# Kernel optimization log

Measured on AMD Instinct MI355X. Metric: run time of the kernel, lower is better.

Reference implementation:

```python
import jax, jax.numpy as jnp
import numpy as np
import math

V, D, L, M, S, B = 32000, 1024, 4, 4096, 2048, 4


def sinusoidal_positional_encoding(max_seq_len, embedding_dim):
    position = jnp.arange(max_seq_len, dtype=jnp.float32)[:, None]
    div_term = jnp.exp(jnp.arange(0, embedding_dim, 2, dtype=jnp.float32)
                       * (-math.log(10000.0) / embedding_dim))
    pe = jnp.zeros((max_seq_len, embedding_dim), jnp.float32)
    pe = pe.at[:, 0::2].set(jnp.sin(position * div_term))
    pe = pe.at[:, 1::2].set(jnp.cos(position * div_term))
    return pe


def setup_inputs() -> dict:
    key = jax.random.key(0)
    ks = jax.random.split(key, 12)
    s = 0.02
    return {
        "x": jax.random.randint(ks[0], (B, S), 0, V, dtype=jnp.int64),
        "emb": jax.random.normal(ks[1], (V, D), jnp.float32) * s,
        "pos_enc": sinusoidal_positional_encoding(S, D),
        "wq": jax.random.normal(ks[2], (D, D), jnp.float32) * s,
        "bq": jnp.zeros((D,), jnp.float32),
        "wk": jax.random.normal(ks[3], (D, D), jnp.float32) * s,
        "bk": jnp.zeros((D,), jnp.float32),
        "wv": jax.random.normal(ks[4], (D, D), jnp.float32) * s,
        "bv": jnp.zeros((D,), jnp.float32),
        "w1s": jax.random.normal(ks[5], (L, D, M), jnp.float32) * s,
        "b1s": jnp.zeros((L, M), jnp.float32),
        "w2s": jax.random.normal(ks[6], (L, M, D), jnp.float32) * s,
        "b2s": jnp.zeros((L, D), jnp.float32),
    }


def reference(x, emb, pos_enc, wq, bq, wk, bk, wv, bv, w1s, b1s, w2s, b2s):
    seq = x.shape[1]
    h = emb[x] + pos_enc[:seq]                      # [B,S,D]
    q = h @ wq + bq
    k = h @ wk + bk
    v = h @ wv + bv
    scores = jnp.einsum('bqd,bkd->bqk', q, k) / jnp.sqrt(jnp.float32(k.shape[-1]))
    # Faithful to source: triu(diagonal=0) KEPT -> attends to self and future.
    mask = jnp.triu(jnp.ones((seq, seq), bool), k=0)
    scores = jnp.where(mask, scores, -jnp.inf)
    attn = jax.nn.softmax(scores, axis=-1)
    h = jax.nn.relu(jnp.einsum('bqk,bkd->bqd', attn, v))
    for i in range(w1s.shape[0]):
        h = jax.nn.relu(h @ w1s[i] + b1s[i])
        h = jax.nn.relu(h @ w2s[i] + b2s[i])
    return h
```

## Files before the change

kernel.cpp:

```cpp
#include <hip/hip_runtime.h>

#define D_DIM 1024
#define S_DIM 2048
#define B_DIM 4
#define M_DIM 4096
#define NTOK  8192

typedef unsigned short u16;
typedef __attribute__((ext_vector_type(8))) short short8;
typedef __attribute__((ext_vector_type(4))) float fx4;

static __device__ __forceinline__ float b2f(u16 u) {
  union { unsigned int i; float f; } v; v.i = ((unsigned int)u) << 16; return v.f;
}
static __device__ __forceinline__ u16 f2b(float f) {
  union { float f; unsigned int i; } v; v.f = f;
  unsigned int r = v.i + 0x7fffu + ((v.i >> 16) & 1u);
  return (u16)(r >> 16);
}
static __device__ __forceinline__ void async16(u16* lds, const u16* g) {
  __builtin_amdgcn_global_load_lds(
      (__attribute__((address_space(1))) void*)(u16*)g,
      (__attribute__((address_space(3))) void*)lds, 16, 0, 0);
}

__global__ void canary_kernel(float* __restrict__ out) {
  const long i = ((long)blockIdx.x * 256 + threadIdx.x) * 4;
  float4 v = {1.0f, 1.0f, 1.0f, 1.0f};
  *(float4*)(out + i) = v;
}

__global__ void Transformer_33792802685820_kernel(
    const int* __restrict__ x, const float* __restrict__ emb,
    const float* __restrict__ pe, u16* __restrict__ h) {
  const int t = blockIdx.x;
  const int s = t & (S_DIM - 1);
  const int row = x[t];
  const int d = threadIdx.x * 4;
  float4 e = *(const float4*)(emb + (long)row * D_DIM + d);
  float4 p = *(const float4*)(pe + (long)s * D_DIM + d);
  ushort4 o;
  o.x = f2b(e.x + p.x);
  o.y = f2b(e.y + p.y);
  o.z = f2b(e.z + p.z);
  o.w = f2b(e.w + p.w);
  *(ushort4*)(h + (long)t * D_DIM + d) = o;
}

__global__ void transpose_f_kernel(
    const float* __restrict__ in, u16* __restrict__ out, int R, int C) {
  __shared__ float tile[32][33];
  const int c0 = blockIdx.x * 32, r0 = blockIdx.y * 32;
  const int tx = threadIdx.x, ty = threadIdx.y;
  for (int i = ty; i < 32; i += 8)
    tile[i][tx] = in[(long)(r0 + i) * C + (c0 + tx)];
  __syncthreads();
  for (int i = ty; i < 32; i += 8)
    out[(long)(c0 + i) * R + (r0 + tx)] = f2b(tile[tx][i]);
}

__global__ void transpose_b_kernel(
    const u16* __restrict__ in, u16* __restrict__ out, int R, int C) {
  __shared__ u16 tile[32][33];
  const long zoff = (long)blockIdx.z * R * C;
  const int c0 = blockIdx.x * 32, r0 = blockIdx.y * 32;
  const int tx = threadIdx.x, ty = threadIdx.y;
  for (int i = ty; i < 32; i += 8)
    tile[i][tx] = in[zoff + (long)(r0 + i) * C + (c0 + tx)];
  __syncthreads();
  for (int i = ty; i < 32; i += 8)
    out[zoff + (long)(c0 + i) * R + (r0 + tx)] = tile[tx][i];
}

template<bool RELU, bool BIAS, bool OUTF32>
__global__ void gemm_bt(
    const u16* __restrict__ A, const u16* __restrict__ Bt,
    const float* __restrict__ bias, u16* __restrict__ C, float* __restrict__ Cf,
    int M, int N, int K, float scale, long sA, long sB, long sC) {
  __shared__ u16 As[128 * 32];
  __shared__ u16 Bs[128 * 32];
  const int tid  = threadIdx.x;
  const int wave = tid >> 6;
  const int lane = tid & 63;
  const int quad = lane >> 4;
  const int l16  = lane & 15;
  const int wm = (wave & 1) << 6;
  const int wn = (wave >> 1) << 6;
  A  += (long)blockIdx.z * sA;
  Bt += (long)blockIdx.z * sB;
  const int m0 = blockIdx.y << 7;
  const int n0 = blockIdx.x << 7;

  const int row_a = tid >> 2;
  const int c4    = (tid & 3) << 3;
  const u16* gA = A  + (long)(m0 + row_a) * K + c4;
  const u16* gB = Bt + (long)(n0 + row_a) * K + c4;
  u16* lA = &As[tid * 8];
  u16* lB = &Bs[tid * 8];

  fx4 acc[4][4] = {};

  for (int k0 = 0; k0 < K; k0 += 32) {
    async16(lA,            gA + k0);
    async16(lA + 64 * 32,  gA + (long)64 * K + k0);
    async16(lB,            gB + k0);
    async16(lB + 64 * 32,  gB + (long)64 * K + k0);
    __syncthreads();
    short8 af[4], bfv[4];
    #pragma unroll
    for (int i = 0; i < 4; ++i) {
      af[i]  = *(const short8*)&As[(wm + i * 16 + l16) * 32 + quad * 8];
      bfv[i] = *(const short8*)&Bs[(wn + i * 16 + l16) * 32 + quad * 8];
    }
    __syncthreads();
    #pragma unroll
    for (int mi = 0; mi < 4; ++mi)
      #pragma unroll
      for (int ni = 0; ni < 4; ++ni)
        acc[mi][ni] = __builtin_amdgcn_mfma_f32_16x16x32_bf16(
            af[mi], bfv[ni], acc[mi][ni], 0, 0, 0);
  }

  float bv[4];
  #pragma unroll
  for (int ni = 0; ni < 4; ++ni)
    bv[ni] = BIAS ? bias[n0 + wn + ni * 16 + l16] : 0.0f;

  #pragma unroll
  for (int mi = 0; mi < 4; ++mi) {
    #pragma unroll
    for (int r = 0; r < 4; ++r) {
      const long row = m0 + wm + mi * 16 + quad * 4 + r;
      const long base = row * N + n0 + wn + l16;
      #pragma unroll
      for (int ni = 0; ni < 4; ++ni) {
        float v = acc[mi][ni][r] * scale + bv[ni];
        if (RELU) { if (v < 0.0f) v = 0.0f; }
        if (OUTF32) Cf[(long)blockIdx.z * sC + base + ni * 16] = v;
        else        C [(long)blockIdx.z * sC + base + ni * 16] = f2b(v);
      }
    }
  }
}

__global__ void softmax_kernel(u16* __restrict__ P) {
  const int q = blockIdx.x;
  u16* p = P + ((long)blockIdx.y * S_DIM + q) * S_DIM;
  const int tid = threadIdx.x;
  const int wave = tid >> 6, lane = tid & 63;
  __shared__ float red[4];
  float vals[8];
  float mx = -3.0e38f;
  for (int it = 0; it < 8; ++it) {
    int k = tid + it * 256;
    float v = (k >= q) ? b2f(p[k]) : -3.0e38f;
    vals[it] = v;
    mx = fmaxf(mx, v);
  }
  for (int off = 32; off > 0; off >>= 1)
    mx = fmaxf(mx, __shfl_down(mx, off, 64));
  if (lane == 0) red[wave] = mx;
  __syncthreads();
  mx = fmaxf(fmaxf(red[0], red[1]), fmaxf(red[2], red[3]));
  __syncthreads();
  float sum = 0.0f;
  for (int it = 0; it < 8; ++it) {
    int k = tid + it * 256;
    float e = (k >= q) ? __expf(vals[it] - mx) : 0.0f;
    vals[it] = e;
    sum += e;
  }
  for (int off = 32; off > 0; off >>= 1)
    sum += __shfl_down(sum, off, 64);
  if (lane == 0) red[wave] = sum;
  __syncthreads();
  sum = red[0] + red[1] + red[2] + red[3];
  const float inv = 1.0f / sum;
  for (int it = 0; it < 8; ++it) {
    int k = tid + it * 256;
    p[k] = f2b(vals[it] * inv);
  }
}

extern "C" void kernel_launch(void* const* d_in, const int* in_sizes, int n_in,
                              void* d_out, int out_size, void* d_ws, size_t ws_size,
                              hipStream_t stream) {
  (void)in_sizes; (void)n_in; (void)out_size; (void)ws_size;
  const int*   x   = (const int*)d_in[0];
  const float* emb = (const float*)d_in[1];
  const float* pe  = (const float*)d_in[2];
  const float* wq  = (const float*)d_in[3];
  const float* bq  = (const float*)d_in[4];
  const float* wk  = (const float*)d_in[5];
  const float* bk  = (const float*)d_in[6];
  const float* wv  = (const float*)d_in[7];
  const float* bv  = (const float*)d_in[8];
  const float* w1s = (const float*)d_in[9];
  const float* b1s = (const float*)d_in[10];
  const float* w2s = (const float*)d_in[11];
  const float* b2s = (const float*)d_in[12];
  float* out = (float*)d_out;

  u16* ws  = (u16*)d_ws;
  u16* h   = ws;
  u16* q   = h  + (long)NTOK * D_DIM;
  u16* kx  = q  + (long)NTOK * D_DIM;
  u16* v   = kx + (long)NTOK * D_DIM;
  u16* P   = v  + (long)NTOK * D_DIM;
  u16* wqT = P  + (long)B_DIM * S_DIM * S_DIM;
  u16* wkT = wqT + (long)D_DIM * D_DIM;
  u16* wvT = wkT + (long)D_DIM * D_DIM;
  u16* w1T = wvT + (long)D_DIM * D_DIM;
  u16* w2T = w1T + (long)D_DIM * M_DIM;
  u16* vT  = q;
  u16* mb  = kx;

  const dim3 blk256(256);
  const dim3 blkT(32, 8);

  canary_kernel<<<dim3(NTOK), blk256, 0, stream>>>(out);

  transpose_f_kernel<<<dim3(32, 32), blkT, 0, stream>>>(wq, wqT, 1024, 1024);
  transpose_f_kernel<<<dim3(32, 32), blkT, 0, stream>>>(wk, wkT, 1024, 1024);
  transpose_f_kernel<<<dim3(32, 32), blkT, 0, stream>>>(wv, wvT, 1024, 1024);

  Transformer_33792802685820_kernel<<<dim3(NTOK), blk256, 0, stream>>>(x, emb, pe, h);

  gemm_bt<false, true, false><<<dim3(8, 64, 1), blk256, 0, stream>>>(h, wqT, bq, q,  nullptr, NTOK, D_DIM, D_DIM, 1.0f, 0, 0, 0);
  gemm_bt<false, true, false><<<dim3(8, 64, 1), blk256, 0, stream>>>(h, wkT, bk, kx, nullptr, NTOK, D_DIM, D_DIM, 1.0f, 0, 0, 0);
  gemm_bt<false, true, false><<<dim3(8, 64, 1), blk256, 0, stream>>>(h, wvT, bv, v,  nullptr, NTOK, D_DIM, D_DIM, 1.0f, 0, 0, 0);

  gemm_bt<false, false, false><<<dim3(16, 16, 4), blk256, 0, stream>>>(q, kx, nullptr, P, nullptr,
      S_DIM, S_DIM, D_DIM, 0.03125f, (long)S_DIM * D_DIM, (long)S_DIM * D_DIM, (long)S_DIM * S_DIM);

  softmax_kernel<<<dim3(S_DIM, B_DIM), blk256, 0, stream>>>(P);

  transpose_b_kernel<<<dim3(32, 64, 4), blkT, 0, stream>>>(v, vT, 2048, 1024);
  gemm_bt<true, false, false><<<dim3(8, 16, 4), blk256, 0, stream>>>(P, vT, nullptr, h, nullptr,
      S_DIM, D_DIM, S_DIM, 1.0f, (long)S_DIM * S_DIM, (long)D_DIM * S_DIM, (long)S_DIM * D_DIM);

  for (int i = 0; i < 4; ++i) {
    transpose_f_kernel<<<dim3(128, 32), blkT, 0, stream>>>(w1s + (long)i * D_DIM * M_DIM, w1T, 1024, 4096);
    transpose_f_kernel<<<dim3(32, 128), blkT, 0, stream>>>(w2s + (long)i * D_DIM * M_DIM, w2T, 4096, 1024);
    gemm_bt<true, true, false><<<dim3(32, 64, 1), blk256, 0, stream>>>(
        h, w1T, b1s + i * M_DIM, mb, nullptr, NTOK, M_DIM, D_DIM, 1.0f, 0, 0, 0);
    if (i == 3)
      gemm_bt<true, true, true><<<dim3(8, 64, 1), blk256, 0, stream>>>(
          mb, w2T, b2s + i * D_DIM, nullptr, out, NTOK, D_DIM, M_DIM, 1.0f, 0, 0, 0);
    else
      gemm_bt<true, true, false><<<dim3(8, 64, 1), blk256, 0, stream>>>(
          mb, w2T, b2s + i * D_DIM, h, nullptr, NTOK, D_DIM, M_DIM, 1.0f, 0, 0, 0);
  }
}
```

Baseline: 1.234 ms.

## Add 256x256-tile 512-thread GEMM with ping-pong scheduling for projection and MLP

Adds a new GEMM kernel that computes 256x256 output tiles with 8 waves. It double-buffers LDS through async global-to-LDS loads, uses an XOR-swizzled layout, and interleaves barrier-separated MFMA clusters at raised priority with the next tile's loads. A workgroup remap groups tiles into chunks of eight for cache locality. All QKV, score and MLP GEMMs switch to it to raise arithmetic intensity and overlap memory with compute. The cost is more LDS and registers per block, fewer blocks for the smaller GEMMs, and many barriers.

```diff
diff --git a/kernel.cpp b/kernel.cpp
--- a/kernel.cpp
+++ b/kernel.cpp
@@ -23,6 +23,9 @@
       (__attribute__((address_space(1))) void*)(u16*)g,
       (__attribute__((address_space(3))) void*)lds, 16, 0, 0);
 }
+
+#define FENCE asm volatile("" ::: "memory")
+#define BARR  do { FENCE; __builtin_amdgcn_s_barrier(); FENCE; } while (0)
 
 __global__ void canary_kernel(float* __restrict__ out) {
   const long i = ((long)blockIdx.x * 256 + threadIdx.x) * 4;
@@ -143,6 +146,137 @@
   }
 }
 
+template<bool RELU, bool BIAS, bool OUTF32>
+__global__ __launch_bounds__(512, 2) void gemm256(
+    const u16* __restrict__ A, const u16* __restrict__ Bt,
+    const float* __restrict__ bias, u16* __restrict__ C, float* __restrict__ Cf,
+    int M, int N, int K, float scale, long sA_, long sB_, long sC_) {
+  __shared__ u16 sA[2][256 * 64];
+  __shared__ u16 sB[2][256 * 64];
+  const int tid  = threadIdx.x;
+  const int lane = tid & 63;
+  const int wave = tid >> 6;
+  const int quad = lane >> 4;
+  const int l16  = lane & 15;
+  const int swz  = l16 & 7;
+  const int wm   = wave >> 2;
+  const int wn   = wave & 3;
+
+  const int gx  = gridDim.x;
+  const int nwg = gx * gridDim.y;
+  const int id0 = blockIdx.y * gx + blockIdx.x;
+  const int cpx = nwg >> 3;
+  const int sid = (id0 & 7) * cpx + (id0 >> 3);
+  const int n0  = (sid % gx) << 8;
+  const int m0  = (sid / gx) << 8;
+
+  A  += (long)blockIdx.z * sA_;
+  Bt += (long)blockIdx.z * sB_;
+
+  const int srow = tid >> 3;
+  const int cl   = (tid & 7) ^ (srow & 7);
+  const u16* gA = A  + (long)(m0 + srow) * K + cl * 8;
+  const u16* gB = Bt + (long)(n0 + srow) * K + cl * 8;
+  const int ldst = tid * 8;
+
+  fx4 acc[8][4] = {};
+  short8 ar[4], br[4];
+
+  const int NT = K >> 6;
+
+#define STAGE_A(b, t, half) do { \
+    const long ko_ = (long)(t) * 64; \
+    async16(&sA[b][(half) * 8192 + ldst],        gA + (long)((half) * 128     ) * K + ko_); \
+    async16(&sA[b][(half) * 8192 + 4096 + ldst], gA + (long)((half) * 128 + 64) * K + ko_); \
+  } while (0)
+#define STAGE_B(b, t, half) do { \
+    const long ko_ = (long)(t) * 64; \
+    async16(&sB[b][(half) * 8192 + ldst],        gB + (long)((half) * 128     ) * K + ko_); \
+    async16(&sB[b][(half) * 8192 + 4096 + ldst], gB + (long)((half) * 128 + 64) * K + ko_); \
+  } while (0)
+#define RD_A(b, mh, ks) do { \
+    _Pragma("unroll") for (int i_ = 0; i_ < 4; ++i_) { \
+      const int row_ = wm * 128 + ((mh) * 4 + i_) * 16 + l16; \
+      ar[i_] = *(const short8*)&sA[b][row_ * 64 + ((((ks) << 2) | quad) ^ swz) * 8]; \
+    } } while (0)
+#define RD_B(b, ks) do { \
+    _Pragma("unroll") for (int n_ = 0; n_ < 4; ++n_) { \
+      const int row_ = wn * 64 + n_ * 16 + l16; \
+      br[n_] = *(const short8*)&sB[b][row_ * 64 + ((((ks) << 2) | quad) ^ swz) * 8]; \
+    } } while (0)
+#define MM(mh) do { \
+    _Pragma("unroll") for (int i_ = 0; i_ < 4; ++i_) \
+      _Pragma("unroll") for (int n_ = 0; n_ < 4; ++n_) \
+        acc[(mh) * 4 + i_][n_] = __builtin_amdgcn_mfma_f32_16x16x32_bf16( \
+            ar[i_], br[n_], acc[(mh) * 4 + i_][n_], 0, 0, 0); \
+  } while (0)
+#define MFMA_CLUSTER(mh) do { \
+    __builtin_amdgcn_sched_barrier(0); \
+    __builtin_amdgcn_s_setprio(1); \
+    MM(mh); \
+    __builtin_amdgcn_s_setprio(0); \
+    __builtin_amdgcn_sched_barrier(0); \
+  } while (0)
+
+  STAGE_B(0, 0, 0); STAGE_B(0, 0, 1);
+  STAGE_A(0, 0, 0); STAGE_A(0, 0, 1);
+  STAGE_B(1, 1, 0);
+  asm volatile("s_waitcnt vmcnt(2)" ::: "memory");
+  BARR;
+
+  for (int t = 0; t < NT; ++t) {
+    const int b = t & 1, b1 = b ^ 1;
+    RD_A(b, 0, 0); RD_B(b, 0);
+    if (t + 1 < NT) STAGE_B(b1, t + 1, 1);
+    BARR;
+    MFMA_CLUSTER(0);
+    BARR;
+    RD_A(b, 1, 0);
+    if (t + 1 < NT) STAGE_A(b1, t + 1, 0);
+    BARR;
+    MFMA_CLUSTER(1);
+    BARR;
+    RD_A(b, 0, 1); RD_B(b, 1);
+    if (t + 1 < NT) STAGE_A(b1, t + 1, 1);
+    BARR;
+    MFMA_CLUSTER(0);
+    BARR;
+    RD_A(b, 1, 1);
+    if (t + 2 < NT) STAGE_B(b, t + 2, 0);
+    BARR;
+    MFMA_CLUSTER(1);
+    asm volatile("s_waitcnt vmcnt(2)" ::: "memory");
+    BARR;
+  }
+
+  float bv[4];
+  #pragma unroll
+  for (int n = 0; n < 4; ++n)
+    bv[n] = BIAS ? bias[n0 + wn * 64 + n * 16 + l16] : 0.0f;
+
+  #pragma unroll
+  for (int f = 0; f < 8; ++f) {
+    #pragma unroll
+    for (int r = 0; r < 4; ++r) {
+      const long row  = m0 + wm * 128 + f * 16 + quad * 4 + r;
+      const long base = (long)blockIdx.z * sC_ + row * N + n0 + wn * 64 + l16;
+      #pragma unroll
+      for (int n = 0; n < 4; ++n) {
+        float v = acc[f][n][r] * scale + bv[n];
+        if (RELU) { if (v < 0.0f) v = 0.0f; }
+        if (OUTF32) Cf[base + n * 16] = v;
+        else        C [base + n * 16] = f2b(v);
+      }
+    }
+  }
+#undef STAGE_A
+#undef STAGE_B
+#undef RD_A
+#undef RD_B
+#undef MM
+#undef MFMA_CLUSTER
+}
+
 __global__ void softmax_kernel(u16* __restrict__ P) {
   const int q = blockIdx.x;
   u16* p = P + ((long)blockIdx.y * S_DIM + q) * S_DIM;
@@ -216,6 +350,7 @@
   u16* mb  = kx;
 
   const dim3 blk256(256);
+  const dim3 blk512(512);
   const dim3 blkT(32, 8);
 
   canary_kernel<<<dim3(NTOK), blk256, 0, stream>>>(out);
@@ -226,11 +361,11 @@
 
   Transformer_33792802685820_kernel<<<dim3(NTOK), blk256, 0, stream>>>(x, emb, pe, h);
 
-  gemm_bt<false, true, false><<<dim3(8, 64, 1), blk256, 0, stream>>>(h, wqT, bq, q,  nullptr, NTOK, D_DIM, D_DIM, 1.0f, 0, 0, 0);
-  gemm_bt<false, true, false><<<dim3(8, 64, 1), blk256, 0, stream>>>(h, wkT, bk, kx, nullptr, NTOK, D_DIM, D_DIM, 1.0f, 0, 0, 0);
-  gemm_bt<false, true, false><<<dim3(8, 64, 1), blk256, 0, stream>>>(h, wvT, bv, v,  nullptr, NTOK, D_DIM, D_DIM, 1.0f, 0, 0, 0);
-
-  gemm_bt<false, false, false><<<dim3(16, 16, 4), blk256, 0, stream>>>(q, kx, nullptr, P, nullptr,
+  gemm256<false, true, false><<<dim3(4, 32, 1), blk512, 0, stream>>>(h, wqT, bq, q,  nullptr, NTOK, D_DIM, D_DIM, 1.0f, 0, 0, 0);
+  gemm256<false, true, false><<<dim3(4, 32, 1), blk512, 0, stream>>>(h, wkT, bk, kx, nullptr, NTOK, D_DIM, D_DIM, 1.0f, 0, 0, 0);
+  gemm256<false, true, false><<<dim3(4, 32, 1), blk512, 0, stream>>>(h, wvT, bv, v,  nullptr, NTOK, D_DIM, D_DIM, 1.0f, 0, 0, 0);
+
+  gemm256<false, false, false><<<dim3(8, 8, 4), blk512, 0, stream>>>(q, kx, nullptr, P, nullptr,
       S_DIM, S_DIM, D_DIM, 0.03125f, (long)S_DIM * D_DIM, (long)S_DIM * D_DIM, (long)S_DIM * S_DIM);
 
   softmax_kernel<<<dim3(S_DIM, B_DIM), blk256, 0, stream>>>(P);
@@ -242,13 +377,13 @@
   for (int i = 0; i < 4; ++i) {
     transpose_f_kernel<<<dim3(128, 32), blkT, 0, stream>>>(w1s + (long)i * D_DIM * M_DIM, w1T, 1024, 4096);
     transpose_f_kernel<<<dim3(32, 128), blkT, 0, stream>>>(w2s + (long)i * D_DIM * M_DIM, w2T, 4096, 1024);
-    gemm_bt<true, true, false><<<dim3(32, 64, 1), blk256, 0, stream>>>(
+    gemm256<true, true, false><<<dim3(16, 32, 1), blk512, 0, stream>>>(
         h, w1T, b1s + i * M_DIM, mb, nullptr, NTOK, M_DIM, D_DIM, 1.0f, 0, 0, 0);
     if (i == 3)
-      gemm_bt<true, true, true><<<dim3(8, 64, 1), blk256, 0, stream>>>(
+      gemm256<true, true, true><<<dim3(4, 32, 1), blk512, 0, stream>>>(
           mb, w2T, b2s + i * D_DIM, nullptr, out, NTOK, D_DIM, M_DIM, 1.0f, 0, 0, 0);
     else
-      gemm_bt<true, true, false><<<dim3(8, 64, 1), blk256, 0, stream>>>(
+      gemm256<true, true, false><<<dim3(4, 32, 1), blk512, 0, stream>>>(
           mb, w2T, b2s + i * D_DIM, h, nullptr, NTOK, D_DIM, M_DIM, 1.0f, 0, 0, 0);
   }
 }
```

Result: no change. 1.255 ms (+1.7%).

## Add 256x256-tile 8-wave pipelined GEMM for QK^T and FFN up-projection

Applied to the files above, without the earlier changes.

Introduces a new bf16 MFMA GEMM kernel with 256x256 output tiles, 512 threads, double-buffered LDS filled by async global-to-LDS loads, an interleaved stage/compute schedule with barriers and wave priority boosts, and an XCD-aware block remap. It replaces the 128-tile kernel for the QK^T score GEMM and the FFN first GEMM. The aim is more data reuse per block and load latency hidden behind MFMA work. The cost is fewer blocks, which can leave compute units underfilled on the smaller grids, plus heavy LDS and register use.

```diff
diff --git a/kernel.cpp b/kernel.cpp
--- a/kernel.cpp
+++ b/kernel.cpp
@@ -143,6 +143,141 @@
   }
 }
 
+template<bool RELU, bool BIAS, bool OUTF32>
+__global__ __launch_bounds__(512) void gemm256(
+    const u16* __restrict__ A, const u16* __restrict__ Bt,
+    const float* __restrict__ bias, u16* __restrict__ C, float* __restrict__ Cf,
+    int M, int N, int K, float scale, long sA_, long sB_, long sC_) {
+  __shared__ u16 sA[2][16384];
+  __shared__ u16 sB[2][16384];
+  const int tid  = threadIdx.x;
+  const int lane = tid & 63;
+  const int wave = tid >> 6;
+  const int quad = lane >> 4;
+  const int l16  = lane & 15;
+  const int wm   = wave >> 2;
+  const int wn   = wave & 3;
+
+  const int gx  = gridDim.x;
+  const int nwg = gx * gridDim.y;
+  const int id0 = blockIdx.y * gx + blockIdx.x;
+  const int cpx = nwg >> 3;
+  const int sid = (id0 & 7) * cpx + (id0 >> 3);
+  const int n0  = (sid % gx) << 8;
+  const int m0  = (sid / gx) << 8;
+
+  A  += (long)blockIdx.z * sA_;
+  Bt += (long)blockIdx.z * sB_;
+
+  const int lr   = tid >> 2;
+  const int pc   = tid & 3;
+  const int lc   = pc ^ (lr & 3);
+  const int arow = (lr & 63) + ((lr >> 6) << 7);
+  const u16* gA0 = A  + (long)(m0 + arow) * K + lc * 8;
+  const u16* gB0 = Bt + (long)(n0 + lr)   * K + lc * 8;
+  const int ldst = tid << 3;
+
+  const int rdo = (quad ^ (l16 & 3)) << 3;
+  const int raA = wm * 64 + l16;
+  const int raB = wn * 64 + l16;
+
+  fx4 acc[8][4] = {};
+  short8 ar[4], br[4];
+
+  const int NT = K >> 6;
+
+#define STG_A(b, t, mh, ks) \
+  async16(&sA[b][((((ks) << 1) | (mh)) << 12) + ldst], \
+          gA0 + (long)(mh) * 64 * K + (long)(t) * 64 + (ks) * 32)
+#define STG_B1(b, t, ks) \
+  async16(&sB[b][((ks) << 13) + ldst], gB0 + (long)(t) * 64 + (ks) * 32)
+#define STG_B2(b, t, ks) \
+  async16(&sB[b][((ks) << 13) + 4096 + ldst], \
+          gB0 + (long)128 * K + (long)(t) * 64 + (ks) * 32)
+#define RD_A(b, mh, ks) do { \
+    _Pragma("unroll") for (int i_ = 0; i_ < 4; ++i_) \
+      ar[i_] = *(const short8*)&sA[b][((((ks) << 1) | (mh)) << 12) + (raA + i_ * 16) * 32 + rdo]; \
+  } while (0)
+#define RD_B(b, ks) do { \
+    _Pragma("unroll") for (int n_ = 0; n_ < 4; ++n_) \
+      br[n_] = *(const short8*)&sB[b][((ks) << 13) + (raB + n_ * 16) * 32 + rdo]; \
+  } while (0)
+#define PRIO_MM(mh) do { \
+    __builtin_amdgcn_s_setprio(1); \
+    _Pragma("unroll") for (int i_ = 0; i_ < 4; ++i_) \
+      _Pragma("unroll") for (int n_ = 0; n_ < 4; ++n_) \
+        acc[(mh) * 4 + i_][n_] = __builtin_amdgcn_mfma_f32_16x16x32_bf16( \
+            ar[i_], br[n_], acc[(mh) * 4 + i_][n_], 0, 0, 0); \
+    __builtin_amdgcn_s_setprio(0); \
+  } while (0)
+#define SBAR  __builtin_amdgcn_s_barrier()
+#define SCHED __builtin_amdgcn_sched_barrier(0)
+
+  STG_A(0, 0, 0, 0); STG_B1(0, 0, 0); STG_B2(0, 0, 0); STG_A(0, 0, 1, 0);
+  STG_A(0, 0, 0, 1); STG_B1(0, 0, 1); STG_B2(0, 0, 1); STG_A(0, 0, 1, 1);
+  STG_A(1, 1, 0, 0); STG_B1(1, 1, 0); STG_B2(1, 1, 0); STG_A(1, 1, 1, 0);
+  STG_A(1, 1, 0, 1); STG_B1(1, 1, 1);
+  asm volatile("s_waitcnt vmcnt(6)");
+  SCHED;
+  SBAR;
+
+  for (int t = 0; t < NT; ++t) {
+    const int b = t & 1, b1 = b ^ 1;
+    RD_A(b, 0, 0); RD_B(b, 0);
+    if (t + 1 < NT) { STG_B2(b1, t + 1, 1); STG_A(b1, t + 1, 1, 1); }
+    SBAR;
+    PRIO_MM(0);
+    SBAR; SCHED;
+    RD_A(b, 1, 0);
+    if (t + 2 < NT) { STG_A(b, t + 2, 0, 0); STG_B1(b, t + 2, 0); }
+    SBAR;
+    PRIO_MM(1);
+    SBAR; SCHED;
+    RD_A(b, 0, 1); RD_B(b, 1);
+    if (t + 2 < NT) { STG_B2(b, t + 2, 0); STG_A(b, t + 2, 1, 0); }
+    SBAR;
+    PRIO_MM(0);
+    SBAR; SCHED;
+    RD_A(b, 1, 1);
+    if (t + 2 < NT) { STG_A(b, t + 2, 0, 1); STG_B1(b, t + 2, 1); }
+    SBAR;
+    PRIO_MM(1);
+    if (t + 2 < NT) asm volatile("s_waitcnt vmcnt(6)");
+    else            asm volatile("s_waitcnt vmcnt(0)");
+    SCHED;
+    SBAR; SCHED;
+  }
+
+  float bv[4];
+  #pragma unroll
+  for (int n = 0; n < 4; ++n)
+    bv[n] = BIAS ? bias[n0 + wn * 64 + n * 16 + l16] : 0.0f;
+
+  #pragma unroll
+  for (int f = 0; f < 8; ++f) {
+    #pragma unroll
+    for (int r = 0; r < 4; ++r) {
+      const long row  = m0 + wm * 128 + f * 16 + quad * 4 + r;
+      const long base = (long)blockIdx.z * sC_ + row * N + n0 + wn * 64 + l16;
+      #pragma unroll
+      for (int n = 0; n < 4; ++n) {
+        float v = acc[f][n][r] * scale + bv[n];
+        if (RELU) { if (v < 0.0f) v = 0.0f; }
+        if (OUTF32) Cf[base + n * 16] = v;
+        else        C [base + n * 16] = f2b(v);
+      }
+    }
+  }
+#undef STG_A
+#undef STG_B1
+#undef STG_B2
+#undef RD_A
+#undef RD_B
+#undef PRIO_MM
+#undef SBAR
+#undef SCHED
+}
+
 __global__ void softmax_kernel(u16* __restrict__ P) {
   const int q = blockIdx.x;
   u16* p = P + ((long)blockIdx.y * S_DIM + q) * S_DIM;
@@ -216,6 +351,7 @@
   u16* mb  = kx;
 
   const dim3 blk256(256);
+  const dim3 blk512(512);
   const dim3 blkT(32, 8);
 
   canary_kernel<<<dim3(NTOK), blk256, 0, stream>>>(out);
@@ -230,7 +366,7 @@
   gemm_bt<false, true, false><<<dim3(8, 64, 1), blk256, 0, stream>>>(h, wkT, bk, kx, nullptr, NTOK, D_DIM, D_DIM, 1.0f, 0, 0, 0);
   gemm_bt<false, true, false><<<dim3(8, 64, 1), blk256, 0, stream>>>(h, wvT, bv, v,  nullptr, NTOK, D_DIM, D_DIM, 1.0f, 0, 0, 0);
 
-  gemm_bt<false, false, false><<<dim3(16, 16, 4), blk256, 0, stream>>>(q, kx, nullptr, P, nullptr,
+  gemm256<false, false, false><<<dim3(8, 8, 4), blk512, 0, stream>>>(q, kx, nullptr, P, nullptr,
       S_DIM, S_DIM, D_DIM, 0.03125f, (long)S_DIM * D_DIM, (long)S_DIM * D_DIM, (long)S_DIM * S_DIM);
 
   softmax_kernel<<<dim3(S_DIM, B_DIM), blk256, 0, stream>>>(P);
@@ -242,7 +378,7 @@
   for (int i = 0; i < 4; ++i) {
     transpose_f_kernel<<<dim3(128, 32), blkT, 0, stream>>>(w1s + (long)i * D_DIM * M_DIM, w1T, 1024, 4096);
     transpose_f_kernel<<<dim3(32, 128), blkT, 0, stream>>>(w2s + (long)i * D_DIM * M_DIM, w2T, 4096, 1024);
-    gemm_bt<true, true, false><<<dim3(32, 64, 1), blk256, 0, stream>>>(
+    gemm256<true, true, false><<<dim3(16, 32, 1), blk512, 0, stream>>>(
         h, w1T, b1s + i * M_DIM, mb, nullptr, NTOK, M_DIM, D_DIM, 1.0f, 0, 0, 0);
     if (i == 3)
       gemm_bt<true, true, true><<<dim3(8, 64, 1), blk256, 0, stream>>>(
```

New measurement: 1.240 ms. No clear change (+0.4%).

## Replace GEMM with 256-row double-buffered swizzled LDS kernel using 512 threads

Applied to the files above, without the earlier changes.

Replaces the 128x128, BK=32, single-buffered GEMM with a 256xBN (BN 128/256), BK=64 tile kernel run by 512 threads. It double-buffers LDS with async global-to-LDS loads, uses an XOR swizzle on LDS columns to avoid bank conflicts, raises wave priority around the MFMA bursts, and remaps block IDs so neighbouring tiles are grouped (intended for XCD/L2 locality). The goal is higher arithmetic intensity and overlap of loads with MFMA work across all the GEMMs. The cost is much larger LDS use (up to 128KB per block), which lowers occupancy, and the grid remap assumes the block count divides by 8.

```diff
diff --git a/kernel.cpp b/kernel.cpp
--- a/kernel.cpp
+++ b/kernel.cpp
@@ -72,75 +72,123 @@
     out[zoff + (long)(c0 + i) * R + (r0 + tx)] = tile[tx][i];
 }
 
-template<bool RELU, bool BIAS, bool OUTF32>
-__global__ void gemm_bt(
+template<int BN, bool RELU, bool BIAS, bool OUTF32>
+__global__ __launch_bounds__(512) void gemm256(
     const u16* __restrict__ A, const u16* __restrict__ Bt,
     const float* __restrict__ bias, u16* __restrict__ C, float* __restrict__ Cf,
-    int M, int N, int K, float scale, long sA, long sB, long sC) {
-  __shared__ u16 As[128 * 32];
-  __shared__ u16 Bs[128 * 32];
+    int M, int N, int K, float scale, long sA_, long sB_, long sC_) {
+  static_assert(BN == 256 || BN == 128, "BN");
+  constexpr int WN   = BN / 64;
+  constexpr int WM   = 8 / WN;
+  constexpr int MF   = 256 / (WM * 16);
+  constexpr int NB_B = BN / 64;
+
+  __shared__ u16 sA0[256 * 64];
+  __shared__ u16 sA1[256 * 64];
+  __shared__ u16 sB0[BN * 64];
+  __shared__ u16 sB1[BN * 64];
+
   const int tid  = threadIdx.x;
+  const int lane = tid & 63;
   const int wave = tid >> 6;
-  const int lane = tid & 63;
   const int quad = lane >> 4;
   const int l16  = lane & 15;
-  const int wm = (wave & 1) << 6;
-  const int wn = (wave >> 1) << 6;
-  A  += (long)blockIdx.z * sA;
-  Bt += (long)blockIdx.z * sB;
-  const int m0 = blockIdx.y << 7;
-  const int n0 = blockIdx.x << 7;
-
-  const int row_a = tid >> 2;
-  const int c4    = (tid & 3) << 3;
-  const u16* gA = A  + (long)(m0 + row_a) * K + c4;
-  const u16* gB = Bt + (long)(n0 + row_a) * K + c4;
-  u16* lA = &As[tid * 8];
-  u16* lB = &Bs[tid * 8];
-
-  fx4 acc[4][4] = {};
-
-  for (int k0 = 0; k0 < K; k0 += 32) {
-    async16(lA,            gA + k0);
-    async16(lA + 64 * 32,  gA + (long)64 * K + k0);
-    async16(lB,            gB + k0);
-    async16(lB + 64 * 32,  gB + (long)64 * K + k0);
-    __syncthreads();
-    short8 af[4], bfv[4];
-    #pragma unroll
-    for (int i = 0; i < 4; ++i) {
-      af[i]  = *(const short8*)&As[(wm + i * 16 + l16) * 32 + quad * 8];
-      bfv[i] = *(const short8*)&Bs[(wn + i * 16 + l16) * 32 + quad * 8];
-    }
-    __syncthreads();
-    #pragma unroll
-    for (int mi = 0; mi < 4; ++mi)
-      #pragma unroll
-      for (int ni = 0; ni < 4; ++ni)
-        acc[mi][ni] = __builtin_amdgcn_mfma_f32_16x16x32_bf16(
-            af[mi], bfv[ni], acc[mi][ni], 0, 0, 0);
+  const int wm   = wave / WN;
+  const int wn   = wave % WN;
+
+  const int gx  = gridDim.x;
+  const int nwg = gx * gridDim.y;
+  const int id0 = blockIdx.y * gx + blockIdx.x;
+  const int cpx = nwg >> 3;
+  const int sid = (id0 & 7) * cpx + (id0 >> 3);
+  const int n0  = (sid % gx) * BN;
+  const int m0  = (sid / gx) << 8;
+
+  A  += (long)blockIdx.z * sA_;
+  Bt += (long)blockIdx.z * sB_;
+
+  const int srow = tid >> 3;
+  const int pc   = tid & 7;
+  const int lc   = pc ^ (srow & 7);
+  const u16* gA0 = A  + (long)(m0 + srow) * K + lc * 8;
+  const u16* gB0 = Bt + (long)(n0 + srow) * K + lc * 8;
+  const int ldst = tid << 3;
+
+  fx4 acc[MF][4] = {};
+
+  const int NT = K >> 6;
+
+#define STG(Sa, Sb, t) do { \
+    const long ko_ = (long)(t) << 6; \
+    _Pragma("unroll") for (int bb_ = 0; bb_ < 4; ++bb_) \
+      async16(&Sa[bb_ * 4096 + ldst], gA0 + (long)(bb_ * 64) * K + ko_); \
+    _Pragma("unroll") for (int bb_ = 0; bb_ < NB_B; ++bb_) \
+      async16(&Sb[bb_ * 4096 + ldst], gB0 + (long)(bb_ * 64) * K + ko_); \
+  } while (0)
+
+#define HALF(Sa, Sb) do { \
+    _Pragma("unroll") for (int ks_ = 0; ks_ < 2; ++ks_) { \
+      const int cko_ = ((((ks_) << 2) | quad) ^ (l16 & 7)) << 3; \
+      short8 ar_[MF], br_[4]; \
+      _Pragma("unroll") for (int i_ = 0; i_ < MF; ++i_) { \
+        const int r_ = wm * (MF * 16) + i_ * 16 + l16; \
+        ar_[i_] = *(const short8*)&Sa[(r_ >> 6) * 4096 + (r_ & 63) * 64 + cko_]; \
+      } \
+      _Pragma("unroll") for (int n_ = 0; n_ < 4; ++n_) { \
+        const int r_ = wn * 64 + n_ * 16 + l16; \
+        br_[n_] = *(const short8*)&Sb[(r_ >> 6) * 4096 + (r_ & 63) * 64 + cko_]; \
+      } \
+      __builtin_amdgcn_s_setprio(1); \
+      _Pragma("unroll") for (int i_ = 0; i_ < MF; ++i_) \
+        _Pragma("unroll") for (int n_ = 0; n_ < 4; ++n_) \
+          acc[i_][n_] = __builtin_amdgcn_mfma_f32_16x16x32_bf16( \
+              ar_[i_], br_[n_], acc[i_][n_], 0, 0, 0); \
+      __builtin_amdgcn_s_setprio(0); \
+    } \
+  } while (0)
+
+#define TILE_END do { \
+    __builtin_amdgcn_sched_barrier(0); \
+    asm volatile("s_waitcnt vmcnt(0)"); \
+    __builtin_amdgcn_s_barrier(); \
+    __builtin_amdgcn_sched_barrier(0); \
+  } while (0)
+
+  STG(sA0, sB0, 0);
+  TILE_END;
+
+  for (int t = 0; t < NT; t += 2) {
+    STG(sA1, sB1, t + 1);
+    HALF(sA0, sB0);
+    TILE_END;
+    if (t + 2 < NT) STG(sA0, sB0, t + 2);
+    HALF(sA1, sB1);
+    TILE_END;
   }
 
   float bv[4];
   #pragma unroll
-  for (int ni = 0; ni < 4; ++ni)
-    bv[ni] = BIAS ? bias[n0 + wn + ni * 16 + l16] : 0.0f;
+  for (int n = 0; n < 4; ++n)
+    bv[n] = BIAS ? bias[n0 + wn * 64 + n * 16 + l16] : 0.0f;
 
   #pragma unroll
-  for (int mi = 0; mi < 4; ++mi) {
+  for (int f = 0; f < MF; ++f) {
     #pragma unroll
     for (int r = 0; r < 4; ++r) {
-      const long row = m0 + wm + mi * 16 + quad * 4 + r;
-      const long base = row * N + n0 + wn + l16;
+      const long row  = m0 + wm * (MF * 16) + f * 16 + quad * 4 + r;
+      const long base = (long)blockIdx.z * sC_ + row * N + n0 + wn * 64 + l16;
       #pragma unroll
-      for (int ni = 0; ni < 4; ++ni) {
-        float v = acc[mi][ni][r] * scale + bv[ni];
+      for (int n = 0; n < 4; ++n) {
+        float v = acc[f][n][r] * scale + bv[n];
         if (RELU) { if (v < 0.0f) v = 0.0f; }
-        if (OUTF32) Cf[(long)blockIdx.z * sC + base + ni * 16] = v;
-        else        C [(long)blockIdx.z * sC + base + ni * 16] = f2b(v);
+        if (OUTF32) Cf[base + n * 16] = v;
+        else        C [base + n * 16] = f2b(v);
       }
     }
   }
+#undef STG
+#undef HALF
+#undef TILE_END
 }
 
 __global__ void softmax_kernel(u16* __restrict__ P) {
@@ -216,6 +264,7 @@
   u16* mb  = kx;
 
   const dim3 blk256(256);
+  const dim3 blk512(512);
   const dim3 blkT(32, 8);
 
   canary_kernel<<<dim3(NTOK), blk256, 0, stream>>>(out);
@@ -226,29 +275,29 @@
 
   Transformer_33792802685820_kernel<<<dim3(NTOK), blk256, 0, stream>>>(x, emb, pe, h);
 
-  gemm_bt<false, true, false><<<dim3(8, 64, 1), blk256, 0, stream>>>(h, wqT, bq, q,  nullptr, NTOK, D_DIM, D_DIM, 1.0f, 0, 0, 0);
-  gemm_bt<false, true, false><<<dim3(8, 64, 1), blk256, 0, stream>>>(h, wkT, bk, kx, nullptr, NTOK, D_DIM, D_DIM, 1.0f, 0, 0, 0);
-  gemm_bt<false, true, false><<<dim3(8, 64, 1), blk256, 0, stream>>>(h, wvT, bv, v,  nullptr, NTOK, D_DIM, D_DIM, 1.0f, 0, 0, 0);
-
-  gemm_bt<false, false, false><<<dim3(16, 16, 4), blk256, 0, stream>>>(q, kx, nullptr, P, nullptr,
+  gemm256<128, false, true, false><<<dim3(8, 32, 1), blk512, 0, stream>>>(h, wqT, bq, q,  nullptr, NTOK, D_DIM, D_DIM, 1.0f, 0, 0, 0);
+  gemm256<128, false, true, false><<<dim3(8, 32, 1), blk512, 0, stream>>>(h, wkT, bk, kx, nullptr, NTOK, D_DIM, D_DIM, 1.0f, 0, 0, 0);
+  gemm256<128, false, true, false><<<dim3(8, 32, 1), blk512, 0, stream>>>(h, wvT, bv, v,  nullptr, NTOK, D_DIM, D_DIM, 1.0f, 0, 0, 0);
+
+  gemm256<256, false, false, false><<<dim3(8, 8, 4), blk512, 0, stream>>>(q, kx, nullptr, P, nullptr,
       S_DIM, S_DIM, D_DIM, 0.03125f, (long)S_DIM * D_DIM, (long)S_DIM * D_DIM, (long)S_DIM * S_DIM);
 
   softmax_kernel<<<dim3(S_DIM, B_DIM), blk256, 0, stream>>>(P);
 
   transpose_b_kernel<<<dim3(32, 64, 4), blkT, 0, stream>>>(v, vT, 2048, 1024);
-  gemm_bt<true, false, false><<<dim3(8, 16, 4), blk256, 0, stream>>>(P, vT, nullptr, h, nullptr,
+  gemm256<128, true, false, false><<<dim3(8, 8, 4), blk512, 0, stream>>>(P, vT, nullptr, h, nullptr,
       S_DIM, D_DIM, S_DIM, 1.0f, (long)S_DIM * S_DIM, (long)D_DIM * S_DIM, (long)S_DIM * D_DIM);
 
   for (int i = 0; i < 4; ++i) {
     transpose_f_kernel<<<dim3(128, 32), blkT, 0, stream>>>(w1s + (long)i * D_DIM * M_DIM, w1T, 1024, 4096);
     transpose_f_kernel<<<dim3(32, 128), blkT, 0, stream>>>(w2s + (long)i * D_DIM * M_DIM, w2T, 4096, 1024);
-    gemm_bt<true, true, false><<<dim3(32, 64, 1), blk256, 0, stream>>>(
+    gemm256<256, true, true, false><<<dim3(16, 32, 1), blk512, 0, stream>>>(
         h, w1T, b1s + i * M_DIM, mb, nullptr, NTOK, M_DIM, D_DIM, 1.0f, 0, 0, 0);
     if (i == 3)
-      gemm_bt<true, true, true><<<dim3(8, 64, 1), blk256, 0, stream>>>(
+      gemm256<128, true, true, true><<<dim3(8, 32, 1), blk512, 0, stream>>>(
           mb, w2T, b2s + i * D_DIM, nullptr, out, NTOK, D_DIM, M_DIM, 1.0f, 0, 0, 0);
     else
-      gemm_bt<true, true, false><<<dim3(8, 64, 1), blk256, 0, stream>>>(
+      gemm256<128, true, true, false><<<dim3(8, 32, 1), blk512, 0, stream>>>(
           mb, w2T, b2s + i * D_DIM, h, nullptr, NTOK, D_DIM, M_DIM, 1.0f, 0, 0, 0);
   }
 }
```

After: 1.269 ms. 1.03x slower.
